# Optimization experiments

Hardware: AMD Instinct MI355X
Metric: run time of the kernel (lower is better)

## Reference

```python
import jax, jax.numpy as jnp
import numpy as np

N = 100000   # atoms
E = 1000000  # edges per conv (includes N self loops)
R = 10000    # residues
P = 50000    # correspondence pairs
C = 25       # in_channels
D_IN = 7 + C # local_nn input width
RADII = (5.0, 8.5, 10.0)
EPS = 1e-12


def _init_lin(key, fi, fo):
    kw, kb = jax.random.split(key)
    s = 1.0 / np.sqrt(fi)
    W = jax.random.uniform(kw, (fi, fo), minval=-s, maxval=s, dtype=jnp.float32)
    b = jax.random.uniform(kb, (fo,), minval=-s, maxval=s, dtype=jnp.float32)
    return W, b


def setup_inputs() -> dict:
    key = jax.random.key(0)
    ks = jax.random.split(key, 24)
    x = jax.random.normal(ks[0], (N, C), dtype=jnp.float32)
    pos = jax.random.normal(ks[1], (N, 3), dtype=jnp.float32) * 10.0
    nrm = jax.random.normal(ks[2], (N, 3), dtype=jnp.float32)
    nrm = nrm / jnp.linalg.norm(nrm, axis=1, keepdims=True)

    def make_edges(k):
        rnd = jax.random.randint(k, (2, E - N), 0, N, dtype=jnp.int32)
        loops = jnp.tile(jnp.arange(N, dtype=jnp.int32)[None, :], (2, 1))
        return jnp.concatenate([rnd, loops], axis=1)  # [2, E], self loops appended

    ei2, ei3, ei4 = make_edges(ks[3]), make_edges(ks[4]), make_edges(ks[5])
    atom2res = (jnp.arange(N) * R // N).astype(jnp.int32)  # contiguous atom->residue blocks
    src_idx = jax.random.randint(ks[6], (P,), 0, R, dtype=jnp.int32)
    tgt_idx = jax.random.randint(ks[7], (P,), 0, R, dtype=jnp.int32)

    inp = {"x": x, "pos": pos, "normal": nrm, "ei2": ei2, "ei3": ei3, "ei4": ei4,
           "atom2res": atom2res, "src_idx": src_idx, "tgt_idx": tgt_idx}
    for i, n in enumerate(["c2", "c3", "c4"]):
        W1, b1 = _init_lin(ks[8 + 2 * i], D_IN, D_IN)
        W2, b2 = _init_lin(ks[9 + 2 * i], D_IN, 128)
        inp[n + "_W1"], inp[n + "_b1"] = W1, b1
        inp[n + "_W2"], inp[n + "_b2"] = W2, b2
    inp["Wa"], inp["ba"] = _init_lin(ks[14], 384, 256)
    inp["Wr"], inp["br"] = _init_lin(ks[15], 256, 512)
    inp["Wl"], inp["bl"] = _init_lin(ks[16], 512, 1)
    return inp


def _angle(a, b):
    # torch_geometric get_angle: atan2(||cross||, dot); eps keeps grad finite at 0
    cr = jnp.cross(a, b)
    return jnp.arctan2(jnp.sqrt(jnp.sum(cr * cr, axis=1) + EPS), jnp.sum(a * b, axis=1))


def _ppf_conv(x, pos, normal, ei, radius, W1, b1, W2, b2):
    j, i = ei[0], ei[1]  # source, target
    d = pos[j] - pos[i]                                   # [E,3]
    dist = jnp.sqrt(jnp.sum(d * d, axis=1) + EPS)
    a1 = _angle(normal[i], d)
    a2 = _angle(normal[j], d)
    a3 = _angle(normal[i], normal[j])
    ppf = jnp.stack([dist / radius,
                     jnp.sin(a1), jnp.cos(a1),
                     jnp.sin(a2), jnp.cos(a2),
                     jnp.sin(a3), jnp.cos(a3)], axis=1)   # [E,7]
    msg = jnp.concatenate([x[j], ppf], axis=1)            # [E, 7+C]
    h = jnp.tanh(msg @ W1 + b1)                           # local_nn layer 1 (Dropout: eval)
    h = jnp.tanh(h @ W2 + b2)                             # local_nn layer 2 -> [E,128]
    return jax.ops.segment_max(h, i, num_segments=pos.shape[0])  # max aggr


def reference(x, pos, normal, ei2, ei3, ei4, atom2res, src_idx, tgt_idx,
              c2_W1, c2_b1, c2_W2, c2_b2,
              c3_W1, c3_b1, c3_W2, c3_b2,
              c4_W1, c4_b1, c4_W2, c4_b2,
              Wa, ba, Wr, br, Wl, bl):
    o2 = _ppf_conv(x, pos, normal, ei2, RADII[0], c2_W1, c2_b1, c2_W2, c2_b2)
    o3 = _ppf_conv(x, pos, normal, ei3, RADII[1], c3_W1, c3_b1, c3_W2, c3_b2)
    o4 = _ppf_conv(x, pos, normal, ei4, RADII[2], c4_W1, c4_b1, c4_W2, c4_b2)
    atom = jnp.tanh(jnp.concatenate([o2, o3, o4], axis=1) @ Wa + ba)   # [N,256]
    res = jax.ops.segment_max(atom, atom2res, num_segments=R)          # global_max_pool
    res = jnp.tanh(res @ Wr + br)                                      # [R,512]
    out = (res[src_idx] - res[tgt_idx]) @ Wl + bl                      # [P,1] logits
    return out
```

## Files before the change

### kernel.cpp

```cpp
#include <hip/hip_runtime.h>
#include <hip/hip_bf16.h>

#define NN 100000
#define EE 1000000
#define RR 10000
#define PP 50000

typedef _Float16 f16x8 __attribute__((ext_vector_type(8)));
typedef float f32x4 __attribute__((ext_vector_type(4)));
typedef unsigned long long ull;

__device__ __forceinline__ float tfast(float x){
    float e = __expf(2.0f * x);
    return 1.0f - __fdividef(2.0f, e + 1.0f);
}
__device__ __forceinline__ unsigned encf(float f){
    unsigned u = __float_as_uint(f);
    return (u & 0x80000000u) ? ~u : (u | 0x80000000u);
}
__device__ __forceinline__ float decf(unsigned u){
    return (u & 0x80000000u) ? __uint_as_float(u ^ 0x80000000u) : __uint_as_float(~u);
}
__device__ __forceinline__ unsigned pk2(float a, float b){
    _Float16 ha = (_Float16)a, hb = (_Float16)b;
    unsigned short ua = __builtin_bit_cast(unsigned short, ha);
    unsigned short ub = __builtin_bit_cast(unsigned short, hb);
    return (unsigned)ua | ((unsigned)ub << 16);
}
__device__ __forceinline__ ull pk4(float a, float b, float c, float d){
    return ((ull)pk2(c, d) << 32) | (ull)pk2(a, b);
}

__global__ __launch_bounds__(256) void k_xw1(
    const float* __restrict__ x,
    const float* __restrict__ W1_0, const float* __restrict__ b1_0,
    const float* __restrict__ W1_1, const float* __restrict__ b1_1,
    const float* __restrict__ W1_2, const float* __restrict__ b1_2,
    _Float16* __restrict__ xw1)
{
    int g = blockIdx.x * 256 + threadIdx.x;
    if (g >= 3 * NN * 8) return;
    int cv  = g / (NN * 8);
    int rem = g - cv * (NN * 8);
    int n   = rem >> 3, cg = rem & 7;
    const float* W1 = (cv == 0) ? W1_0 : ((cv == 1) ? W1_1 : W1_2);
    const float* b1 = (cv == 0) ? b1_0 : ((cv == 1) ? b1_1 : b1_2);
    float4 acc = *(const float4*)&b1[cg * 4];
    const float* xr = x + (size_t)n * 25;
    #pragma unroll
    for (int m = 0; m < 25; m++){
        float xv = xr[m];
        float4 w = *(const float4*)&W1[m * 32 + cg * 4];
        acc.x = fmaf(xv, w.x, acc.x); acc.y = fmaf(xv, w.y, acc.y);
        acc.z = fmaf(xv, w.z, acc.z); acc.w = fmaf(xv, w.w, acc.w);
    }
    *(ull*)&xw1[((size_t)cv * NN + n) * 32 + cg * 4] = pk4(acc.x, acc.y, acc.z, acc.w);
}

__global__ __launch_bounds__(256) void k_prep(const float* __restrict__ Wa, _Float16* __restrict__ BF)
{
    int g = blockIdx.x * 256 + threadIdx.x;
    int o = g * 4;
    int j0 = o & 7;
    int t1 = o >> 3;
    int ln = t1 & 15;
    int t2 = t1 >> 4;
    int kg = t2 & 3;
    int t3 = t2 >> 2;
    int c  = t3 % 12;
    int nt = t3 / 12;
    int colg = nt * 16 + ln;
    int krow = c * 32 + kg * 8 + j0;
    float w0 = Wa[(size_t)(krow + 0) * 256 + colg];
    float w1 = Wa[(size_t)(krow + 1) * 256 + colg];
    float w2 = Wa[(size_t)(krow + 2) * 256 + colg];
    float w3 = Wa[(size_t)(krow + 3) * 256 + colg];
    *(ull*)&BF[o] = pk4(w0, w1, w2, w3);
}

__global__ __launch_bounds__(256) void k_hist(
    const int* __restrict__ e2, const int* __restrict__ e3, const int* __restrict__ e4,
    unsigned* __restrict__ cur)
{
    long g = (long)blockIdx.x * 256 + threadIdx.x;
    if (g >= 3L * EE) return;
    int cv = (int)(g / EE);
    int e  = (int)(g - (long)cv * EE);
    const int* ei = (cv == 0) ? e2 : ((cv == 1) ? e3 : e4);
    int tg = ei[EE + e];
    atomicAdd(&cur[cv * NN + tg], 1u);
}

__global__ __launch_bounds__(1024) void k_scan(unsigned* __restrict__ cur)
{
    int cv = blockIdx.x;
    unsigned* a = cur + (size_t)cv * NN;
    __shared__ unsigned wsum[16];
    __shared__ unsigned carry;
    if (threadIdx.x == 0) carry = 0;
    int lane = threadIdx.x & 63, wv = threadIdx.x >> 6;
    for (int base = 0; base < NN; base += 1024){
        int idx = base + threadIdx.x;
        unsigned v = (idx < NN) ? a[idx] : 0u;
        unsigned s = v;
        #pragma unroll
        for (int d = 1; d < 64; d <<= 1){
            unsigned t = (unsigned)__shfl_up((int)s, d);
            if (lane >= d) s += t;
        }
        if (lane == 63) wsum[wv] = s;
        __syncthreads();
        if (wv == 0 && lane < 16){
            unsigned t = wsum[lane];
            #pragma unroll
            for (int d = 1; d < 16; d <<= 1){
                unsigned u = (unsigned)__shfl_up((int)t, d);
                if (lane >= d) t += u;
            }
            wsum[lane] = t;
        }
        __syncthreads();
        unsigned waveoff = (wv == 0) ? 0u : wsum[wv - 1];
        unsigned excl = carry + waveoff + s - v;
        if (idx < NN) a[idx] = excl;
        __syncthreads();
        if (threadIdx.x == 0) carry += wsum[15];
        __syncthreads();
    }
}

__global__ __launch_bounds__(256) void k_scatter(
    const int* __restrict__ e2, const int* __restrict__ e3, const int* __restrict__ e4,
    unsigned* __restrict__ cur, int* __restrict__ srcS, int* __restrict__ tgtS)
{
    long g = (long)blockIdx.x * 256 + threadIdx.x;
    if (g >= 3L * EE) return;
    int cv = (int)(g / EE);
    int e  = (int)(g - (long)cv * EE);
    const int* ei = (cv == 0) ? e2 : ((cv == 1) ? e3 : e4);
    int j  = ei[e];
    int tg = ei[EE + e];
    unsigned p = atomicAdd(&cur[cv * NN + tg], 1u);
    srcS[(size_t)cv * EE + p] = j;
    tgtS[(size_t)cv * EE + p] = tg;
}

__global__ __launch_bounds__(256) void k_conv(
    const int* __restrict__ srcS, const int* __restrict__ tgtS,
    const _Float16* __restrict__ xw1,
    const float* __restrict__ pos, const float* __restrict__ nrm,
    const float* __restrict__ W1_0, const float* __restrict__ W1_1, const float* __restrict__ W1_2,
    const float* __restrict__ W2_0, const float* __restrict__ W2_1, const float* __restrict__ W2_2,
    const float* __restrict__ b2_0, const float* __restrict__ b2_1, const float* __restrict__ b2_2,
    unsigned* __restrict__ feat)
{
    const int cv = blockIdx.y;
    const float invR = (cv == 0) ? 0.2f : ((cv == 1) ? (1.0f / 8.5f) : 0.1f);
    const float* W1 = (cv == 0) ? W1_0 : ((cv == 1) ? W1_1 : W1_2);
    const float* W2 = (cv == 0) ? W2_0 : ((cv == 1) ? W2_1 : W2_2);
    const float* b2 = (cv == 0) ? b2_0 : ((cv == 1) ? b2_1 : b2_2);
    const int* sS_g = srcS + (size_t)cv * EE;
    const int* tS_g = tgtS + (size_t)cv * EE;
    const _Float16* xw = xw1 + (size_t)cv * NN * 32;

    __shared__ __align__(16) _Float16 hS[128 * 32];
    __shared__ __align__(16) _Float16 sLds[128 * 128];
    __shared__ float w1p[224];
    __shared__ int tgtL[128];

    int tid = threadIdx.x;
    if (tid < 224) w1p[tid] = W1[800 + tid];

    int gbase = blockIdx.x * 128;
    int e     = tid & 127;
    int hlf   = tid >> 7;
    int eg = gbase + e; if (eg >= EE) eg = EE - 1;
    int j = sS_g[eg], it = tS_g[eg];
    if (hlf == 0) tgtL[e] = it;
    __syncthreads();

    float pix = pos[(size_t)it * 3 + 0], piy = pos[(size_t)it * 3 + 1], piz = pos[(size_t)it * 3 + 2];
    float pjx = pos[(size_t)j  * 3 + 0], pjy = pos[(size_t)j  * 3 + 1], pjz = pos[(size_t)j  * 3 + 2];
    float nix = nrm[(size_t)it * 3 + 0], niy = nrm[(size_t)it * 3 + 1], niz = nrm[(size_t)it * 3 + 2];
    float njx = nrm[(size_t)j  * 3 + 0], njy = nrm[(size_t)j  * 3 + 1], njz = nrm[(size_t)j  * 3 + 2];

    float dx = pjx - pix, dy = pjy - piy, dz = pjz - piz;
    float dist = sqrtf(dx * dx + dy * dy + dz * dz + 1e-12f);

    float cx = niy * dz - niz * dy, cyv = niz * dx - nix * dz, cz = nix * dy - niy * dx;
    float y1 = sqrtf(cx * cx + cyv * cyv + cz * cz + 1e-12f);
    float x1 = nix * dx + niy * dy + niz * dz;
    float ir = __frsqrt_rn(x1 * x1 + y1 * y1);
    float s1 = y1 * ir, c1 = x1 * ir;
    cx = njy * dz - njz * dy; cyv = njz * dx - njx * dz; cz = njx * dy - njy * dx;
    float y2 = sqrtf(cx * cx + cyv * cyv + cz * cz + 1e-12f);
    float x2 = njx * dx + njy * dy + njz * dz;
    ir = __frsqrt_rn(x2 * x2 + y2 * y2);
    float s2 = y2 * ir, c2 = x2 * ir;
    cx = niy * njz - niz * njy; cyv = niz * njx - nix * njz; cz = nix * njy - niy * njx;
    float y3 = sqrtf(cx * cx + cyv * cyv + cz * cz + 1e-12f);
    float x3 = nix * njx + niy * njy + niz * njz;
    ir = __frsqrt_rn(x3 * x3 + y3 * y3);
    float s3 = y3 * ir, c3 = x3 * ir;

    float ppf[7] = { dist * invR, s1, c1, s2, c2, s3, c3 };

    int ch0 = hlf * 16;
    float h16[16];
    {
        const f16x8* xr = (const f16x8*)(xw + (size_t)j * 32 + ch0);
        f16x8 v0 = xr[0], v1 = xr[1];
        #pragma unroll
        for (int q = 0; q < 8; q++){ h16[q] = (float)v0[q]; h16[8 + q] = (float)v1[q]; }
    }
    #pragma unroll
    for (int f = 0; f < 7; f++){
        float pv = ppf[f];
        const float4* w4 = (const float4*)&w1p[f * 32 + ch0];
        #pragma unroll
        for (int q = 0; q < 4; q++){
            float4 w = w4[q];
            h16[q*4+0] = fmaf(pv, w.x, h16[q*4+0]);
            h16[q*4+1] = fmaf(pv, w.y, h16[q*4+1]);
            h16[q*4+2] = fmaf(pv, w.z, h16[q*4+2]);
            h16[q*4+3] = fmaf(pv, w.w, h16[q*4+3]);
        }
    }
    #pragma unroll
    for (int c = 0; c < 16; c++) h16[c] = tfast(h16[c]);

    {
        f16x8 c0v, c1v;
        #pragma unroll
        for (int q = 0; q < 8; q++){ c0v[q] = (_Float16)h16[q]; c1v[q] = (_Float16)h16[8 + q]; }
        int key = (e >> 1) & 3;
        int kg0 = 2 * hlf;
        *(f16x8*)&hS[e * 32 + ((kg0     ) ^ key) * 8] = c0v;
        *(f16x8*)&hS[e * 32 + ((kg0 + 1) ^ key) * 8] = c1v;
    }
    __syncthreads();

    int lane = tid & 63, wv = tid >> 6;
    int ln15 = lane & 15, kg = lane >> 4;
    f16x8 a[8];
    #pragma unroll
    for (int mt = 0; mt < 8; mt++){
        #pragma unroll
        for (int jj = 0; jj < 8; jj++)
            a[mt][jj] = (_Float16)W2[(kg * 8 + jj) * 128 + mt * 16 + ln15];
    }
    f32x4 acc[2][8];
    #pragma unroll
    for (int n = 0; n < 2; n++)
        #pragma unroll
        for (int mt = 0; mt < 8; mt++)
            acc[n][mt] = (f32x4){0.f, 0.f, 0.f, 0.f};

    #pragma unroll
    for (int nti = 0; nti < 2; nti++){
        int ee = (2 * wv + nti) * 16 + ln15;
        f16x8 b = *(const f16x8*)&hS[ee * 32 + (kg ^ ((ee >> 1) & 3)) * 8];
        #pragma unroll
        for (int mt = 0; mt < 8; mt++)
            acc[nti][mt] = __builtin_amdgcn_mfma_f32_16x16x32_f16(a[mt], b, acc[nti][mt], 0, 0, 0);
    }
    #pragma unroll
    for (int nti = 0; nti < 2; nti++){
        int ee  = (2 * wv + nti) * 16 + ln15;
        int key = ee & 15;
        #pragma unroll
        for (int mt = 0; mt < 8; mt++){
            unsigned lo = pk2(acc[nti][mt][0], acc[nti][mt][1]);
            unsigned hi = pk2(acc[nti][mt][2], acc[nti][mt][3]);
            int u = mt * 4 + kg;
            ull v = ((ull)hi << 32) | lo;
            *(ull*)&sLds[ee * 128 + ((u ^ key) << 2)] = v;
        }
    }
    __syncthreads();

    int g  = tid >> 7;
    int c  = tid & 127;
    float b2c = b2[c];
    int cur = -1; float m = -3.0e38f;
    int ebase = g * 64;
    for (int er = 0; er < 64; er++){
        int ee = ebase + er;
        int tg = tgtL[ee];
        float s = (float)sLds[ee * 128 + ((((c >> 2) ^ (ee & 15))) << 2) + (c & 3)];
        if (tg != cur){
            if (cur >= 0)
                atomicMax(&feat[(size_t)cur * 384 + cv * 128 + c], encf(m + b2c));
            cur = tg; m = s;
        } else {
            m = fmaxf(m, s);
        }
    }
    atomicMax(&feat[(size_t)cur * 384 + cv * 128 + c], encf(m + b2c));
}

__global__ __launch_bounds__(256) void k_atom(
    const unsigned* __restrict__ feat, const _Float16* __restrict__ BF,
    const float* __restrict__ ba, float* __restrict__ resm)
{
    __shared__ __align__(16) char ldsbuf[81920];
    _Float16* Ah = (_Float16*)ldsbuf;
    float*    Cs = (float*)ldsbuf;

    int tid = threadIdx.x;
    size_t base = (size_t)blockIdx.x * 80 * 384;

    #pragma unroll
    for (int itr = 0; itr < 30; itr++){
        int idx = itr * 1024 + tid * 4;
        uint4 v = *(const uint4*)&feat[base + idx];
        int r = idx / 384;
        int k = idx - r * 384;
        float f0 = tfast(decf(v.x));
        float f1 = tfast(decf(v.y));
        float f2 = tfast(decf(v.z));
        float f3 = tfast(decf(v.w));
        int u = (k >> 3) ^ (r & 7);
        *(ull*)&Ah[r * 384 + u * 8 + (k & 7)] = pk4(f0, f1, f2, f3);
    }
    __syncthreads();

    int lane = tid & 63, wv = tid >> 6;
    int ln15 = lane & 15, kg = lane >> 4;
    f32x4 acc[5][4];
    #pragma unroll
    for (int mt = 0; mt < 5; mt++)
        #pragma unroll
        for (int nti = 0; nti < 4; nti++)
            acc[mt][nti] = (f32x4){0.f, 0.f, 0.f, 0.f};

    const f16x8* bfp = (const f16x8*)BF;
    #pragma unroll
    for (int c = 0; c < 12; c++){
        f16x8 af[5];
        #pragma unroll
        for (int mt = 0; mt < 5; mt++){
            int row = mt * 16 + ln15;
            af[mt] = *(const f16x8*)&Ah[row * 384 + (((c * 4 + kg) ^ (row & 7)) << 3)];
        }
        #pragma unroll
        for (int nti = 0; nti < 4; nti++){
            f16x8 b = bfp[(((wv * 4 + nti) * 12 + c) * 4 + kg) * 16 + ln15];
            #pragma unroll
            for (int mt = 0; mt < 5; mt++)
                acc[mt][nti] = __builtin_amdgcn_mfma_f32_16x16x32_f16(af[mt], b, acc[mt][nti], 0, 0, 0);
        }
    }
    __syncthreads();

    #pragma unroll
    for (int nti = 0; nti < 4; nti++){
        int col = wv * 64 + nti * 16 + ln15;
        float bac = ba[col];
        #pragma unroll
        for (int mt = 0; mt < 5; mt++){
            #pragma unroll
            for (int q = 0; q < 4; q++){
                int row = mt * 16 + kg * 4 + q;
                Cs[row * 256 + (col ^ (kg << 2))] = acc[mt][nti][q] + bac;
            }
        }
    }
    __syncthreads();

    int res0 = blockIdx.x * 8;
    #pragma unroll
    for (int o = 0; o < 8; o++){
        int out = o * 256 + tid;
        int r = out >> 8, cc = out & 255;
        float m = -3.0e38f;
        #pragma unroll
        for (int q = 0; q < 10; q++){
            int row = r * 10 + q;
            m = fmaxf(m, Cs[row * 256 + (cc ^ (((row >> 2) & 3) << 2))]);
        }
        resm[(size_t)(res0 + r) * 256 + cc] = tfast(m);
    }
}

__global__ __launch_bounds__(256) void k_res(
    const float* __restrict__ resm, const float* __restrict__ Wr,
    const float* __restrict__ br, const float* __restrict__ Wl,
    float* __restrict__ lw)
{
    __shared__ __align__(16) float As[16 * 16];
    __shared__ __align__(16) float Ws[16 * 512];
    __shared__ float lwL[16];
    int tid  = threadIdx.x;
    int row0 = blockIdx.x * 16;
    int colg = tid & 127, rowg = tid >> 7;
    int c0 = colg * 4;
    int lane = tid & 63;
    if (tid < 16) lwL[tid] = 0.0f;
    float4 acc[8];
    float4 brv = *(const float4*)&br[c0];
    #pragma unroll
    for (int r = 0; r < 8; r++) acc[r] = brv;

    for (int k0 = 0; k0 < 256; k0 += 16){
        __syncthreads();
        { int r = tid >> 4, k = tid & 15;
          As[tid] = resm[(size_t)(row0 + r) * 256 + k0 + k]; }
        #pragma unroll
        for (int t0 = 0; t0 < 32; t0++){
            int t = tid + t0 * 256;
            int k = t >> 9, c = t & 511;
            Ws[t] = Wr[(size_t)(k0 + k) * 512 + c];
        }
        __syncthreads();
        #pragma unroll
        for (int kk = 0; kk < 16; kk += 4){
            float4 w0 = *(const float4*)&Ws[(kk + 0) * 512 + c0];
            float4 w1 = *(const float4*)&Ws[(kk + 1) * 512 + c0];
            float4 w2 = *(const float4*)&Ws[(kk + 2) * 512 + c0];
            float4 w3 = *(const float4*)&Ws[(kk + 3) * 512 + c0];
            #pragma unroll
            for (int r = 0; r < 8; r++){
                const float4 a = *(const float4*)&As[(rowg * 8 + r) * 16 + kk];
                acc[r].x = fmaf(a.x, w0.x, fmaf(a.y, w1.x, fmaf(a.z, w2.x, fmaf(a.w, w3.x, acc[r].x))));
                acc[r].y = fmaf(a.x, w0.y, fmaf(a.y, w1.y, fmaf(a.z, w2.y, fmaf(a.w, w3.y, acc[r].y))));
                acc[r].z = fmaf(a.x, w0.z, fmaf(a.y, w1.z, fmaf(a.z, w2.z, fmaf(a.w, w3.z, acc[r].z))));
                acc[r].w = fmaf(a.x, w0.w, fmaf(a.y, w1.w, fmaf(a.z, w2.w, fmaf(a.w, w3.w, acc[r].w))));
            }
        }
    }
    float4 wl = *(const float4*)&Wl[c0];
    #pragma unroll
    for (int r = 0; r < 8; r++){
        float4 v = acc[r];
        float p = tfast(v.x) * wl.x + tfast(v.y) * wl.y + tfast(v.z) * wl.z + tfast(v.w) * wl.w;
        #pragma unroll
        for (int m = 1; m < 64; m <<= 1) p += __shfl_xor(p, m);
        if (lane == 0) atomicAdd(&lwL[rowg * 8 + r], p);
    }
    __syncthreads();
    if (tid < 16) lw[row0 + tid] = lwL[tid];
}

__global__ __launch_bounds__(256) void k_out(
    const float* __restrict__ lw, const int* __restrict__ src, const int* __restrict__ tgt,
    const float* __restrict__ bl, float* __restrict__ out)
{
    int p = blockIdx.x * 256 + threadIdx.x;
    if (p < PP) out[p] = lw[src[p]] - lw[tgt[p]] + bl[0];
}

extern "C" void kernel_launch(void* const* d_in, const int* in_sizes, int n_in,
                              void* d_out, int out_size, void* d_ws, size_t ws_size,
                              hipStream_t stream)
{
    const float* x    = (const float*)d_in[0];
    const float* pos  = (const float*)d_in[1];
    const float* nrm  = (const float*)d_in[2];
    const int*   ei2  = (const int*)d_in[3];
    const int*   ei3  = (const int*)d_in[4];
    const int*   ei4  = (const int*)d_in[5];
    const int*   srci = (const int*)d_in[7];
    const int*   tgti = (const int*)d_in[8];
    const float* c2W1 = (const float*)d_in[9];
    const float* c2b1 = (const float*)d_in[10];
    const float* c2W2 = (const float*)d_in[11];
    const float* c2b2 = (const float*)d_in[12];
    const float* c3W1 = (const float*)d_in[13];
    const float* c3b1 = (const float*)d_in[14];
    const float* c3W2 = (const float*)d_in[15];
    const float* c3b2 = (const float*)d_in[16];
    const float* c4W1 = (const float*)d_in[17];
    const float* c4b1 = (const float*)d_in[18];
    const float* c4W2 = (const float*)d_in[19];
    const float* c4b2 = (const float*)d_in[20];
    const float* Wa   = (const float*)d_in[21];
    const float* ba   = (const float*)d_in[22];
    const float* Wr   = (const float*)d_in[23];
    const float* br   = (const float*)d_in[24];
    const float* Wl   = (const float*)d_in[25];
    const float* bl   = (const float*)d_in[26];

    char* ws = (char*)d_ws;
    _Float16* xw1  = (_Float16*)(ws);
    _Float16* BF   = (_Float16*)(ws +  19200000);
    unsigned* cur  = (unsigned*)(ws +  19396608);
    int*      srcS = (int*)     (ws +  20596736);
    int*      tgtS = (int*)     (ws +  32596736);
    unsigned* feat = (unsigned*)(ws +  44596736);
    float*    resm = (float*)   (ws + 198196736);
    float*    lw   = (float*)   (ws + 208436736);

    hipMemsetAsync(cur,  0, (size_t)3 * NN * 4, stream);
    hipMemsetAsync(feat, 0, (size_t)NN * 384 * 4, stream);

    k_xw1<<<9375, 256, 0, stream>>>(x, c2W1, c2b1, c3W1, c3b1, c4W1, c4b1, xw1);
    k_prep<<<96, 256, 0, stream>>>(Wa, BF);
    k_hist<<<(3 * EE + 255) / 256, 256, 0, stream>>>(ei2, ei3, ei4, cur);
    k_scan<<<3, 1024, 0, stream>>>(cur);
    k_scatter<<<(3 * EE + 255) / 256, 256, 0, stream>>>(ei2, ei3, ei4, cur, srcS, tgtS);
    dim3 gconv((EE + 127) / 128, 3);
    k_conv<<<gconv, 256, 0, stream>>>(srcS, tgtS, xw1, pos, nrm,
                                      c2W1, c3W1, c4W1, c2W2, c3W2, c4W2,
                                      c2b2, c3b2, c4b2, feat);
    k_atom<<<NN / 80, 256, 0, stream>>>(feat, BF, ba, resm);
    k_res<<<RR / 16, 256, 0, stream>>>(resm, Wr, br, Wl, lw);
    k_out<<<(PP + 255) / 256, 256, 0, stream>>>(lw, srci, tgti, bl, (float*)d_out);
}
```

Before: 992.0 us.

## Pack sorted edges into 64-bit words, prepack W2 fragments, vectorize max-reduction

```diff
diff --git a/kernel.cpp b/kernel.cpp
--- a/kernel.cpp
+++ b/kernel.cpp
@@ -7,6 +7,7 @@
 #define PP 50000
 
 typedef _Float16 f16x8 __attribute__((ext_vector_type(8)));
+typedef _Float16 f16x2 __attribute__((ext_vector_type(2)));
 typedef float f32x4 __attribute__((ext_vector_type(4)));
 typedef unsigned long long ull;
 
@@ -78,6 +79,24 @@
     *(ull*)&BF[o] = pk4(w0, w1, w2, w3);
 }
 
+__global__ __launch_bounds__(256) void k_prepw(
+    const float* __restrict__ W2_0, const float* __restrict__ W2_1, const float* __restrict__ W2_2,
+    _Float16* __restrict__ W2F)
+{
+    int g = blockIdx.x * 256 + threadIdx.x;
+    int cv = g >> 9;
+    int f  = g & 511;
+    int ln = f & 15;
+    int kg = (f >> 4) & 3;
+    int mt = f >> 6;
+    const float* W2 = (cv == 0) ? W2_0 : ((cv == 1) ? W2_1 : W2_2);
+    f16x8 v;
+    #pragma unroll
+    for (int jj = 0; jj < 8; jj++)
+        v[jj] = (_Float16)W2[(kg * 8 + jj) * 128 + mt * 16 + ln];
+    ((f16x8*)W2F)[g] = v;
+}
+
 __global__ __launch_bounds__(256) void k_hist(
     const int* __restrict__ e2, const int* __restrict__ e3, const int* __restrict__ e4,
     unsigned* __restrict__ cur)
@@ -131,7 +150,7 @@
 
 __global__ __launch_bounds__(256) void k_scatter(
     const int* __restrict__ e2, const int* __restrict__ e3, const int* __restrict__ e4,
-    unsigned* __restrict__ cur, int* __restrict__ srcS, int* __restrict__ tgtS)
+    unsigned* __restrict__ cur, ull* __restrict__ esort)
 {
     long g = (long)blockIdx.x * 256 + threadIdx.x;
     if (g >= 3L * EE) return;
@@ -141,26 +160,23 @@
     int j  = ei[e];
     int tg = ei[EE + e];
     unsigned p = atomicAdd(&cur[cv * NN + tg], 1u);
-    srcS[(size_t)cv * EE + p] = j;
-    tgtS[(size_t)cv * EE + p] = tg;
+    esort[(size_t)cv * EE + p] = ((ull)(unsigned)tg << 32) | (unsigned)j;
 }
 
 __global__ __launch_bounds__(256) void k_conv(
-    const int* __restrict__ srcS, const int* __restrict__ tgtS,
+    const ull* __restrict__ esort,
     const _Float16* __restrict__ xw1,
     const float* __restrict__ pos, const float* __restrict__ nrm,
     const float* __restrict__ W1_0, const float* __restrict__ W1_1, const float* __restrict__ W1_2,
-    const float* __restrict__ W2_0, const float* __restrict__ W2_1, const float* __restrict__ W2_2,
+    const _Float16* __restrict__ W2F,
     const float* __restrict__ b2_0, const float* __restrict__ b2_1, const float* __restrict__ b2_2,
     unsigned* __restrict__ feat)
 {
     const int cv = blockIdx.y;
     const float invR = (cv == 0) ? 0.2f : ((cv == 1) ? (1.0f / 8.5f) : 0.1f);
     const float* W1 = (cv == 0) ? W1_0 : ((cv == 1) ? W1_1 : W1_2);
-    const float* W2 = (cv == 0) ? W2_0 : ((cv == 1) ? W2_1 : W2_2);
     const float* b2 = (cv == 0) ? b2_0 : ((cv == 1) ? b2_1 : b2_2);
-    const int* sS_g = srcS + (size_t)cv * EE;
-    const int* tS_g = tgtS + (size_t)cv * EE;
+    const ull* eS = esort + (size_t)cv * EE;
     const _Float16* xw = xw1 + (size_t)cv * NN * 32;
 
     __shared__ __align__(16) _Float16 hS[128 * 32];
@@ -175,7 +191,9 @@
     int e     = tid & 127;
     int hlf   = tid >> 7;
     int eg = gbase + e; if (eg >= EE) eg = EE - 1;
-    int j = sS_g[eg], it = tS_g[eg];
+    ull ev = eS[eg];
+    int j  = (int)(unsigned)(ev & 0xffffffffu);
+    int it = (int)(unsigned)(ev >> 32);
     if (hlf == 0) tgtL[e] = it;
     __syncthreads();
 
@@ -242,13 +260,12 @@
 
     int lane = tid & 63, wv = tid >> 6;
     int ln15 = lane & 15, kg = lane >> 4;
+    const f16x8* w2f = (const f16x8*)W2F + (size_t)cv * 512;
     f16x8 a[8];
     #pragma unroll
-    for (int mt = 0; mt < 8; mt++){
-        #pragma unroll
-        for (int jj = 0; jj < 8; jj++)
-            a[mt][jj] = (_Float16)W2[(kg * 8 + jj) * 128 + mt * 16 + ln15];
-    }
+    for (int mt = 0; mt < 8; mt++)
+        a[mt] = w2f[(mt * 4 + kg) * 16 + ln15];
+
     f32x4 acc[2][8];
     #pragma unroll
     for (int n = 0; n < 2; n++)
@@ -279,24 +296,40 @@
     }
     __syncthreads();
 
-    int g  = tid >> 7;
-    int c  = tid & 127;
-    float b2c = b2[c];
-    int cur = -1; float m = -3.0e38f;
-    int ebase = g * 64;
-    for (int er = 0; er < 64; er++){
+    int egp = tid >> 5;
+    int cg  = tid & 31;
+    float4 b2v = *(const float4*)&b2[cg * 4];
+    int curT = -1;
+    f16x2 m01 = (f16x2)(_Float16)(-60000.0f), m23 = m01;
+    int ebase = egp * 16;
+    #pragma unroll
+    for (int er = 0; er < 16; er++){
         int ee = ebase + er;
         int tg = tgtL[ee];
-        float s = (float)sLds[ee * 128 + ((((c >> 2) ^ (ee & 15))) << 2) + (c & 3)];
-        if (tg != cur){
-            if (cur >= 0)
-                atomicMax(&feat[(size_t)cur * 384 + cv * 128 + c], encf(m + b2c));
-            cur = tg; m = s;
+        ull sv = *(const ull*)&sLds[ee * 128 + ((cg ^ er) << 2)];
+        f16x2 s01 = __builtin_bit_cast(f16x2, (unsigned)(sv & 0xffffffffu));
+        f16x2 s23 = __builtin_bit_cast(f16x2, (unsigned)(sv >> 32));
+        if (tg != curT){
+            if (curT >= 0){
+                unsigned* fp = &feat[(size_t)curT * 384 + cv * 128 + cg * 4];
+                atomicMax(fp + 0, encf((float)m01[0] + b2v.x));
+                atomicMax(fp + 1, encf((float)m01[1] + b2v.y));
+                atomicMax(fp + 2, encf((float)m23[0] + b2v.z));
+                atomicMax(fp + 3, encf((float)m23[1] + b2v.w));
+            }
+            curT = tg; m01 = s01; m23 = s23;
         } else {
-            m = fmaxf(m, s);
-        }
-    }
-    atomicMax(&feat[(size_t)cur * 384 + cv * 128 + c], encf(m + b2c));
+            m01 = __builtin_elementwise_max(m01, s01);
+            m23 = __builtin_elementwise_max(m23, s23);
+        }
+    }
+    {
+        unsigned* fp = &feat[(size_t)curT * 384 + cv * 128 + cg * 4];
+        atomicMax(fp + 0, encf((float)m01[0] + b2v.x));
+        atomicMax(fp + 1, encf((float)m01[1] + b2v.y));
+        atomicMax(fp + 2, encf((float)m23[0] + b2v.z));
+        atomicMax(fp + 3, encf((float)m23[1] + b2v.w));
+    }
 }
 
 __global__ __launch_bounds__(256) void k_atom(
@@ -483,25 +516,26 @@
 
     char* ws = (char*)d_ws;
     _Float16* xw1  = (_Float16*)(ws);
-    _Float16* BF   = (_Float16*)(ws +  19200000);
-    unsigned* cur  = (unsigned*)(ws +  19396608);
-    int*      srcS = (int*)     (ws +  20596736);
-    int*      tgtS = (int*)     (ws +  32596736);
-    unsigned* feat = (unsigned*)(ws +  44596736);
-    float*    resm = (float*)   (ws + 198196736);
-    float*    lw   = (float*)   (ws + 208436736);
+    _Float16* W2F  = (_Float16*)(ws +  19200000);
+    _Float16* BF   = (_Float16*)(ws +  19224576);
+    unsigned* cur  = (unsigned*)(ws +  19421184);
+    ull*      esort= (ull*)     (ws +  20621312);
+    unsigned* feat = (unsigned*)(ws +  44621312);
+    float*    resm = (float*)   (ws + 198221312);
+    float*    lw   = (float*)   (ws + 208461312);
 
     hipMemsetAsync(cur,  0, (size_t)3 * NN * 4, stream);
     hipMemsetAsync(feat, 0, (size_t)NN * 384 * 4, stream);
 
     k_xw1<<<9375, 256, 0, stream>>>(x, c2W1, c2b1, c3W1, c3b1, c4W1, c4b1, xw1);
     k_prep<<<96, 256, 0, stream>>>(Wa, BF);
+    k_prepw<<<6, 256, 0, stream>>>(c2W2, c3W2, c4W2, W2F);
     k_hist<<<(3 * EE + 255) / 256, 256, 0, stream>>>(ei2, ei3, ei4, cur);
     k_scan<<<3, 1024, 0, stream>>>(cur);
-    k_scatter<<<(3 * EE + 255) / 256, 256, 0, stream>>>(ei2, ei3, ei4, cur, srcS, tgtS);
+    k_scatter<<<(3 * EE + 255) / 256, 256, 0, stream>>>(ei2, ei3, ei4, cur, esort);
     dim3 gconv((EE + 127) / 128, 3);
-    k_conv<<<gconv, 256, 0, stream>>>(srcS, tgtS, xw1, pos, nrm,
-                                      c2W1, c3W1, c4W1, c2W2, c3W2, c4W2,
+    k_conv<<<gconv, 256, 0, stream>>>(esort, xw1, pos, nrm,
+                                      c2W1, c3W1, c4W1, W2F,
                                       c2b2, c3b2, c4b2, feat);
     k_atom<<<NN / 80, 256, 0, stream>>>(feat, BF, ba, resm);
     k_res<<<RR / 16, 256, 0, stream>>>(resm, Wr, br, Wl, lw);
```

Result: slower. 1.353 ms (+36.4%).
